# Kernel tuning notes

Hardware: AMD Instinct MI355X
Metric: run time of the kernel (lower is better)

The kernel has to match this reference:

```python
import jax, jax.numpy as jnp
import numpy as np

N_NODES = 100000
N_EDGES = 1600000
IN_CH = 256
HID = 64
N_FACTORS = 3
N_SKILLS = 7
NEG_SLOPE = 0.2  # PyG GATConv default leaky-relu slope


def setup_inputs() -> dict:
    key = jax.random.key(0)
    ks = jax.random.split(key, 16)
    def w(k, shape, fan_in):
        return jax.random.normal(k, shape, jnp.float32) * (1.0 / np.sqrt(fan_in))
    return {
        "x": jax.random.normal(ks[0], (N_NODES, IN_CH), jnp.float32),
        "edge_index": jax.random.randint(ks[1], (2, N_EDGES), 0, N_NODES, jnp.int32),
        # GAT layer 1
        "W1": w(ks[2], (IN_CH, HID), IN_CH),
        "a_src1": w(ks[3], (HID,), HID),
        "a_dst1": w(ks[4], (HID,), HID),
        "b1": jnp.zeros((HID,), jnp.float32),
        # GAT layer 2
        "W2": w(ks[5], (HID, HID), HID),
        "a_src2": w(ks[6], (HID,), HID),
        "a_dst2": w(ks[7], (HID,), HID),
        "b2": jnp.zeros((HID,), jnp.float32),
        # heads
        "Wf": w(ks[8], (HID, N_FACTORS), HID),
        "bf": jnp.zeros((N_FACTORS,), jnp.float32),
        "Ws": w(ks[9], (HID, N_SKILLS), HID),
        "bs": jnp.zeros((N_SKILLS,), jnp.float32),
    }


def _gat_layer(x, src, dst, W, a_src, a_dst, b):
    """Single-head GATConv (PyG defaults: heads=1, self-loops already appended)."""
    n = x.shape[0]
    h = x @ W                                     # [N, H] transformed features
    alpha_s = h @ a_src                           # [N] per-node source score
    alpha_d = h @ a_dst                           # [N] per-node destination score
    e = jax.nn.leaky_relu(alpha_s[src] + alpha_d[dst], NEG_SLOPE)  # [E]
    # numerically stable segment softmax over incoming edges of each dst node
    m = jax.ops.segment_max(e, dst, num_segments=n)
    w = jnp.exp(e - m[dst])
    den = jax.ops.segment_sum(w, dst, num_segments=n)
    alpha = w / den[dst]                          # [E] attention coefficients
    out = jax.ops.segment_sum(alpha[:, None] * h[src], dst, num_segments=n)
    return out + b


def reference(x, edge_index, W1, a_src1, a_dst1, b1, W2, a_src2, a_dst2, b2, Wf, bf, Ws, bs):
    n = x.shape[0]
    # GATConv default add_self_loops=True
    loops = jnp.arange(n, dtype=edge_index.dtype)
    src = jnp.concatenate([edge_index[0], loops])
    dst = jnp.concatenate([edge_index[1], loops])

    h = jax.nn.relu(_gat_layer(x, src, dst, W1, a_src1, a_dst1, b1))
    # dropout is identity in eval mode
    h = jax.nn.relu(_gat_layer(h, src, dst, W2, a_src2, a_dst2, b2))

    factors_logits = h @ Wf + bf   # [N, 3]
    skills_logits = h @ Ws + bs    # [N, 7]
    return (factors_logits, skills_logits)
```

## Files before the change

kernel.cpp:

```cpp
#include <hip/hip_runtime.h>

__global__ __launch_bounds__(256) void init_deg(int* deg, int N) {
    int i = blockIdx.x * blockDim.x + threadIdx.x;
    if (i < N) deg[i] = 1;
}

__global__ __launch_bounds__(256) void count_deg_r(const int* __restrict__ edst,
                                                   int* __restrict__ deg, int E,
                                                   float inv, int per_chunk) {
    int r = blockIdx.x & 7;
    int chunk = blockIdx.x >> 3;
    int base = chunk * per_chunk;
    int end = min(E, base + per_chunk);
    for (int e = base + (int)threadIdx.x; e < end; e += 256) {
        int d = edst[e];
        int reg = (int)((float)d * inv); reg = reg > 7 ? 7 : reg;
        if (reg == r) atomicAdd(&deg[d], 1);
    }
}

__global__ __launch_bounds__(256) void scan_pass1(const int* __restrict__ deg,
                                                  int* __restrict__ partials, int N) {
    __shared__ int sd[256];
    int b = blockIdx.x, t = threadIdx.x;
    int base = b * 1024 + t * 4;
    int s = 0;
#pragma unroll
    for (int k = 0; k < 4; k++) s += (base + k < N) ? deg[base + k] : 0;
    sd[t] = s; __syncthreads();
    for (int off = 1; off < 256; off <<= 1) {
        int v = (t >= off) ? sd[t - off] : 0;
        __syncthreads();
        sd[t] += v;
        __syncthreads();
    }
    if (t == 255) partials[b] = sd[255];
}

__global__ __launch_bounds__(256) void scan_pass2(int* __restrict__ partials, int nblk) {
    __shared__ int sd[256];
    int t = threadIdx.x;
    int v[4]; int s = 0;
#pragma unroll
    for (int k = 0; k < 4; k++) { int i = t * 4 + k; v[k] = (i < nblk) ? partials[i] : 0; s += v[k]; }
    sd[t] = s; __syncthreads();
    for (int off = 1; off < 256; off <<= 1) {
        int x = (t >= off) ? sd[t - off] : 0;
        __syncthreads();
        sd[t] += x;
        __syncthreads();
    }
    int run = sd[t] - s;
#pragma unroll
    for (int k = 0; k < 4; k++) { int i = t * 4 + k; if (i < nblk) partials[i] = run; run += v[k]; }
}

__global__ __launch_bounds__(256) void scan_pass3(const int* __restrict__ deg,
                                                  const int* __restrict__ partials,
                                                  int* __restrict__ rowstart, int N) {
    __shared__ int sd[256];
    int b = blockIdx.x, t = threadIdx.x;
    int base = b * 1024 + t * 4;
    int v[4]; int s = 0;
#pragma unroll
    for (int k = 0; k < 4; k++) { v[k] = (base + k < N) ? deg[base + k] : 0; s += v[k]; }
    sd[t] = s; __syncthreads();
    for (int off = 1; off < 256; off <<= 1) {
        int x = (t >= off) ? sd[t - off] : 0;
        __syncthreads();
        sd[t] += x;
        __syncthreads();
    }
    int run = partials[b] + sd[t] - s;
#pragma unroll
    for (int k = 0; k < 4; k++) { if (base + k < N) rowstart[base + k] = run; run += v[k]; }
}

__global__ __launch_bounds__(256) void scatter_r(const int* __restrict__ esrc,
                                                 const int* __restrict__ edst,
                                                 int* __restrict__ cursor,
                                                 int* __restrict__ sorted_src,
                                                 int E, int total, float inv, int per_chunk) {
    int r = blockIdx.x & 7;
    int chunk = blockIdx.x >> 3;
    int base = chunk * per_chunk;
    int end = min(total, base + per_chunk);
    for (int e = base + (int)threadIdx.x; e < end; e += 256) {
        int s, d;
        if (e < E) { s = esrc[e]; d = edst[e]; }
        else       { s = e - E;   d = s;       }
        int reg = (int)((float)d * inv); reg = reg > 7 ? 7 : reg;
        if (reg == r) {
            int pos = atomicAdd(&cursor[d], 1);
            sorted_src[pos] = s;
        }
    }
}

__global__ __launch_bounds__(256) void gemm_alpha(const float* __restrict__ A,
                                                  const float* __restrict__ W,
                                                  const float* __restrict__ a_src,
                                                  const float* __restrict__ a_dst,
                                                  float* __restrict__ C,
                                                  float* __restrict__ as_,
                                                  float* __restrict__ ad_,
                                                  int M, int K) {
    const int BK = 32;
    __shared__ float AsT[BK][132];
    __shared__ float Bs[BK][64];
    int tid = threadIdx.x;
    int tx = tid & 7;
    int ty = tid >> 3;
    int rowBase = blockIdx.x * 128;
    float acc[4][8] = {};

    float asv[8], adv[8];
#pragma unroll
    for (int j = 0; j < 8; j++) { asv[j] = a_src[tx * 8 + j]; adv[j] = a_dst[tx * 8 + j]; }

    for (int k0 = 0; k0 < K; k0 += BK) {
#pragma unroll
        for (int i = 0; i < 4; i++) {
            int fidx = 4 * (tid + i * 256);
            int r = fidx >> 5, c = fidx & 31;
            int gr = rowBase + r;
            float4 v = (gr < M) ? *reinterpret_cast<const float4*>(&A[(size_t)gr * K + k0 + c])
                                : make_float4(0.f, 0.f, 0.f, 0.f);
            AsT[c + 0][r] = v.x;
            AsT[c + 1][r] = v.y;
            AsT[c + 2][r] = v.z;
            AsT[c + 3][r] = v.w;
        }
#pragma unroll
        for (int i = 0; i < 2; i++) {
            int fidx = 4 * (tid + i * 256);
            int r = fidx >> 6, c = fidx & 63;
            *reinterpret_cast<float4*>(&Bs[r][c]) =
                *reinterpret_cast<const float4*>(&W[(size_t)(k0 + r) * 64 + c]);
        }
        __syncthreads();
#pragma unroll 4
        for (int kk = 0; kk < BK; ++kk) {
            float a[4], b[8];
            *reinterpret_cast<float4*>(&a[0]) = *reinterpret_cast<const float4*>(&AsT[kk][ty * 4]);
            *reinterpret_cast<float4*>(&b[0]) = *reinterpret_cast<const float4*>(&Bs[kk][tx * 8]);
            *reinterpret_cast<float4*>(&b[4]) = *reinterpret_cast<const float4*>(&Bs[kk][tx * 8 + 4]);
#pragma unroll
            for (int i = 0; i < 4; i++)
#pragma unroll
                for (int j = 0; j < 8; j++)
                    acc[i][j] += a[i] * b[j];
        }
        __syncthreads();
    }

#pragma unroll
    for (int i = 0; i < 4; i++) {
        int gr = rowBase + ty * 4 + i;
        float s1 = 0.f, s2 = 0.f;
#pragma unroll
        for (int j = 0; j < 8; j++) { s1 += acc[i][j] * asv[j]; s2 += acc[i][j] * adv[j]; }
        s1 += __shfl_xor(s1, 1); s2 += __shfl_xor(s2, 1);
        s1 += __shfl_xor(s1, 2); s2 += __shfl_xor(s2, 2);
        s1 += __shfl_xor(s1, 4); s2 += __shfl_xor(s2, 4);
        if (gr < M) {
            *reinterpret_cast<float4*>(&C[(size_t)gr * 64 + tx * 8]) =
                make_float4(acc[i][0], acc[i][1], acc[i][2], acc[i][3]);
            *reinterpret_cast<float4*>(&C[(size_t)gr * 64 + tx * 8 + 4]) =
                make_float4(acc[i][4], acc[i][5], acc[i][6], acc[i][7]);
            if (tx == 0) { as_[gr] = s1; ad_[gr] = s2; }
        }
    }
}

__global__ __launch_bounds__(256) void aggregate_kernel(const float* __restrict__ h,
                                                        const float* __restrict__ as_,
                                                        const float* __restrict__ ad_,
                                                        const int* __restrict__ rowstart,
                                                        const int* __restrict__ sorted_src,
                                                        const float* __restrict__ bias,
                                                        float* __restrict__ outp,
                                                        int N, int total) {
    int wid = (blockIdx.x * blockDim.x + threadIdx.x) >> 6;
    int lane = threadIdx.x & 63;
    if (wid >= N) return;
    int beg = rowstart[wid];
    int end = (wid + 1 < N) ? rowstart[wid + 1] : total;
    float a_d = ad_[wid];
    float acc = 0.f, den = 0.f;
    int j = beg;
    for (; j + 3 < end; j += 4) {
        int s0 = sorted_src[j],     s1 = sorted_src[j + 1];
        int s2 = sorted_src[j + 2], s3 = sorted_src[j + 3];
        float e0 = as_[s0] + a_d, e1 = as_[s1] + a_d;
        float e2 = as_[s2] + a_d, e3 = as_[s3] + a_d;
        e0 = e0 > 0.f ? e0 : 0.2f * e0;
        e1 = e1 > 0.f ? e1 : 0.2f * e1;
        e2 = e2 > 0.f ? e2 : 0.2f * e2;
        e3 = e3 > 0.f ? e3 : 0.2f * e3;
        float w0 = __expf(e0), w1 = __expf(e1), w2 = __expf(e2), w3 = __expf(e3);
        float h0 = h[(size_t)s0 * 64 + lane];
        float h1 = h[(size_t)s1 * 64 + lane];
        float h2 = h[(size_t)s2 * 64 + lane];
        float h3 = h[(size_t)s3 * 64 + lane];
        den += (w0 + w1) + (w2 + w3);
        acc += (w0 * h0 + w1 * h1) + (w2 * h2 + w3 * h3);
    }
    for (; j < end; j++) {
        int s0 = sorted_src[j];
        float e0 = as_[s0] + a_d;
        e0 = e0 > 0.f ? e0 : 0.2f * e0;
        float w0 = __expf(e0);
        den += w0;
        acc += w0 * h[(size_t)s0 * 64 + lane];
    }
    float v = acc / den + bias[lane];
    outp[(size_t)wid * 64 + lane] = v > 0.f ? v : 0.f;
}

__global__ __launch_bounds__(256) void aggregate_heads(const float* __restrict__ h,
                                                       const float* __restrict__ as_,
                                                       const float* __restrict__ ad_,
                                                       const int* __restrict__ rowstart,
                                                       const int* __restrict__ sorted_src,
                                                       const float* __restrict__ bias,
                                                       const float* __restrict__ Wf,
                                                       const float* __restrict__ bf,
                                                       const float* __restrict__ Ws,
                                                       const float* __restrict__ bs,
                                                       float* __restrict__ out,
                                                       int N, int total) {
    int wid = (blockIdx.x * blockDim.x + threadIdx.x) >> 6;
    int lane = threadIdx.x & 63;
    if (wid >= N) return;
    int beg = rowstart[wid];
    int end = (wid + 1 < N) ? rowstart[wid + 1] : total;
    float a_d = ad_[wid];
    float acc = 0.f, den = 0.f;
    int j = beg;
    for (; j + 3 < end; j += 4) {
        int s0 = sorted_src[j],     s1 = sorted_src[j + 1];
        int s2 = sorted_src[j + 2], s3 = sorted_src[j + 3];
        float e0 = as_[s0] + a_d, e1 = as_[s1] + a_d;
        float e2 = as_[s2] + a_d, e3 = as_[s3] + a_d;
        e0 = e0 > 0.f ? e0 : 0.2f * e0;
        e1 = e1 > 0.f ? e1 : 0.2f * e1;
        e2 = e2 > 0.f ? e2 : 0.2f * e2;
        e3 = e3 > 0.f ? e3 : 0.2f * e3;
        float w0 = __expf(e0), w1 = __expf(e1), w2 = __expf(e2), w3 = __expf(e3);
        float h0 = h[(size_t)s0 * 64 + lane];
        float h1 = h[(size_t)s1 * 64 + lane];
        float h2 = h[(size_t)s2 * 64 + lane];
        float h3 = h[(size_t)s3 * 64 + lane];
        den += (w0 + w1) + (w2 + w3);
        acc += (w0 * h0 + w1 * h1) + (w2 * h2 + w3 * h3);
    }
    for (; j < end; j++) {
        int s0 = sorted_src[j];
        float e0 = as_[s0] + a_d;
        e0 = e0 > 0.f ? e0 : 0.2f * e0;
        float w0 = __expf(e0);
        den += w0;
        acc += w0 * h[(size_t)s0 * 64 + lane];
    }
    float v = acc / den + bias[lane];
    v = v > 0.f ? v : 0.f;
#pragma unroll
    for (int q = 0; q < 3; q++) {
        float p = v * Wf[lane * 3 + q];
#pragma unroll
        for (int off = 32; off; off >>= 1) p += __shfl_xor(p, off);
        if (lane == 0) out[(size_t)wid * 3 + q] = p + bf[q];
    }
#pragma unroll
    for (int q = 0; q < 7; q++) {
        float p = v * Ws[lane * 7 + q];
#pragma unroll
        for (int off = 32; off; off >>= 1) p += __shfl_xor(p, off);
        if (lane == 0) out[(size_t)N * 3 + (size_t)wid * 7 + q] = p + bs[q];
    }
}

extern "C" void kernel_launch(void* const* d_in, const int* in_sizes, int n_in,
                              void* d_out, int out_size, void* d_ws, size_t ws_size,
                              hipStream_t stream) {
    const float* x      = (const float*)d_in[0];
    const int*   ei     = (const int*)  d_in[1];
    const float* W1     = (const float*)d_in[2];
    const float* a_src1 = (const float*)d_in[3];
    const float* a_dst1 = (const float*)d_in[4];
    const float* b1     = (const float*)d_in[5];
    const float* W2     = (const float*)d_in[6];
    const float* a_src2 = (const float*)d_in[7];
    const float* a_dst2 = (const float*)d_in[8];
    const float* b2     = (const float*)d_in[9];
    const float* Wf     = (const float*)d_in[10];
    const float* bf     = (const float*)d_in[11];
    const float* Ws     = (const float*)d_in[12];
    const float* bs     = (const float*)d_in[13];
    float* out = (float*)d_out;

    const int IN = 256;
    int N = in_sizes[0] / IN;
    int E = in_sizes[1] / 2;
    int total = E + N;

    char* ws = (char*)d_ws;
    float* h        = (float*)ws;  ws += (size_t)N * 64 * sizeof(float);
    float* g        = (float*)ws;  ws += (size_t)N * 64 * sizeof(float);
    float* as_      = (float*)ws;  ws += (size_t)N * sizeof(float);
    float* ad_      = (float*)ws;  ws += (size_t)N * sizeof(float);
    int* rowstart   = (int*)ws;    ws += (size_t)(N + 1) * sizeof(int);
    int* cursor     = (int*)ws;    ws += (size_t)N * sizeof(int);
    int* sorted_src = (int*)ws;    ws += (size_t)total * sizeof(int);
    int* partials   = (int*)ws;    ws += 1024 * sizeof(int);

    const int* esrc = ei;
    const int* edst = ei + E;

    float inv = 8.0f / (float)N;
    int nblk = (N + 1023) / 1024;
    int gemmGrid = (N + 127) / 128;
    int aggGrid  = (N * 64 + 255) / 256;
    int pcE = (E + 255) / 256;
    int pcT = (total + 255) / 256;

    init_deg<<<(N + 255) / 256, 256, 0, stream>>>(cursor, N);
    count_deg_r<<<2048, 256, 0, stream>>>(edst, cursor, E, inv, pcE);
    scan_pass1<<<nblk, 256, 0, stream>>>(cursor, partials, N);
    scan_pass2<<<1, 256, 0, stream>>>(partials, nblk);
    scan_pass3<<<nblk, 256, 0, stream>>>(cursor, partials, rowstart, N);
    hipMemcpyAsync(cursor, rowstart, (size_t)N * sizeof(int), hipMemcpyDeviceToDevice, stream);
    scatter_r<<<2048, 256, 0, stream>>>(esrc, edst, cursor, sorted_src, E, total, inv, pcT);

    gemm_alpha<<<gemmGrid, 256, 0, stream>>>(x, W1, a_src1, a_dst1, h, as_, ad_, N, IN);
    aggregate_kernel<<<aggGrid, 256, 0, stream>>>(h, as_, ad_, rowstart, sorted_src, b1, g, N, total);

    gemm_alpha<<<gemmGrid, 256, 0, stream>>>(g, W2, a_src2, a_dst2, h, as_, ad_, N, 64);
    aggregate_heads<<<aggGrid, 256, 0, stream>>>(h, as_, ad_, rowstart, sorted_src, b2,
                                                 Wf, bf, Ws, bs, out, N, total);
}
```

Before: 592.4 us.

## Store transformed features in fp16 and handle self-loops inline in aggregation

GEMM output h is written as half precision and converted back to float in the gather-heavy aggregation kernels, halving feature gather bandwidth. Self-loops are no longer materialized in the CSR; each aggregation computes the self-edge term directly, removing the init kernel, the device memcpy, and N extra scatter entries. The cursor is now zeroed by memset and filled alongside rowstart in the scan. The fp16 storage reduces precision of intermediate features, which risks exceeding the accuracy tolerance.

```diff
diff --git a/kernel.cpp b/kernel.cpp
--- a/kernel.cpp
+++ b/kernel.cpp
@@ -1,9 +1,5 @@
 #include <hip/hip_runtime.h>
-
-__global__ __launch_bounds__(256) void init_deg(int* deg, int N) {
-    int i = blockIdx.x * blockDim.x + threadIdx.x;
-    if (i < N) deg[i] = 1;
-}
+#include <hip/hip_fp16.h>
 
 __global__ __launch_bounds__(256) void count_deg_r(const int* __restrict__ edst,
                                                    int* __restrict__ deg, int E,
@@ -57,7 +53,8 @@
 
 __global__ __launch_bounds__(256) void scan_pass3(const int* __restrict__ deg,
                                                   const int* __restrict__ partials,
-                                                  int* __restrict__ rowstart, int N) {
+                                                  int* __restrict__ rowstart,
+                                                  int* __restrict__ cursor, int N) {
     __shared__ int sd[256];
     int b = blockIdx.x, t = threadIdx.x;
     int base = b * 1024 + t * 4;
@@ -73,22 +70,23 @@
     }
     int run = partials[b] + sd[t] - s;
 #pragma unroll
-    for (int k = 0; k < 4; k++) { if (base + k < N) rowstart[base + k] = run; run += v[k]; }
+    for (int k = 0; k < 4; k++) {
+        if (base + k < N) { rowstart[base + k] = run; cursor[base + k] = run; }
+        run += v[k];
+    }
 }
 
 __global__ __launch_bounds__(256) void scatter_r(const int* __restrict__ esrc,
                                                  const int* __restrict__ edst,
                                                  int* __restrict__ cursor,
                                                  int* __restrict__ sorted_src,
-                                                 int E, int total, float inv, int per_chunk) {
+                                                 int E, float inv, int per_chunk) {
     int r = blockIdx.x & 7;
     int chunk = blockIdx.x >> 3;
     int base = chunk * per_chunk;
-    int end = min(total, base + per_chunk);
+    int end = min(E, base + per_chunk);
     for (int e = base + (int)threadIdx.x; e < end; e += 256) {
-        int s, d;
-        if (e < E) { s = esrc[e]; d = edst[e]; }
-        else       { s = e - E;   d = s;       }
+        int s = esrc[e], d = edst[e];
         int reg = (int)((float)d * inv); reg = reg > 7 ? 7 : reg;
         if (reg == r) {
             int pos = atomicAdd(&cursor[d], 1);
@@ -101,7 +99,7 @@
                                                   const float* __restrict__ W,
                                                   const float* __restrict__ a_src,
                                                   const float* __restrict__ a_dst,
-                                                  float* __restrict__ C,
+                                                  __half* __restrict__ C,
                                                   float* __restrict__ as_,
                                                   float* __restrict__ ad_,
                                                   int M, int K) {
@@ -164,30 +162,35 @@
         s1 += __shfl_xor(s1, 2); s2 += __shfl_xor(s2, 2);
         s1 += __shfl_xor(s1, 4); s2 += __shfl_xor(s2, 4);
         if (gr < M) {
+            __half hb[8];
+#pragma unroll
+            for (int j = 0; j < 8; j++) hb[j] = __float2half(acc[i][j]);
             *reinterpret_cast<float4*>(&C[(size_t)gr * 64 + tx * 8]) =
-                make_float4(acc[i][0], acc[i][1], acc[i][2], acc[i][3]);
-            *reinterpret_cast<float4*>(&C[(size_t)gr * 64 + tx * 8 + 4]) =
-                make_float4(acc[i][4], acc[i][5], acc[i][6], acc[i][7]);
+                *reinterpret_cast<const float4*>(&hb[0]);
             if (tx == 0) { as_[gr] = s1; ad_[gr] = s2; }
         }
     }
 }
 
-__global__ __launch_bounds__(256) void aggregate_kernel(const float* __restrict__ h,
+__global__ __launch_bounds__(256) void aggregate_kernel(const __half* __restrict__ h,
                                                         const float* __restrict__ as_,
                                                         const float* __restrict__ ad_,
                                                         const int* __restrict__ rowstart,
                                                         const int* __restrict__ sorted_src,
                                                         const float* __restrict__ bias,
                                                         float* __restrict__ outp,
-                                                        int N, int total) {
+                                                        int N, int E) {
     int wid = (blockIdx.x * blockDim.x + threadIdx.x) >> 6;
     int lane = threadIdx.x & 63;
     if (wid >= N) return;
     int beg = rowstart[wid];
-    int end = (wid + 1 < N) ? rowstart[wid + 1] : total;
+    int end = (wid + 1 < N) ? rowstart[wid + 1] : E;
     float a_d = ad_[wid];
-    float acc = 0.f, den = 0.f;
+    float es = as_[wid] + a_d;
+    es = es > 0.f ? es : 0.2f * es;
+    float wself = __expf(es);
+    float den = wself;
+    float acc = wself * __half2float(h[(size_t)wid * 64 + lane]);
     int j = beg;
     for (; j + 3 < end; j += 4) {
         int s0 = sorted_src[j],     s1 = sorted_src[j + 1];
@@ -199,10 +202,10 @@
         e2 = e2 > 0.f ? e2 : 0.2f * e2;
         e3 = e3 > 0.f ? e3 : 0.2f * e3;
         float w0 = __expf(e0), w1 = __expf(e1), w2 = __expf(e2), w3 = __expf(e3);
-        float h0 = h[(size_t)s0 * 64 + lane];
-        float h1 = h[(size_t)s1 * 64 + lane];
-        float h2 = h[(size_t)s2 * 64 + lane];
-        float h3 = h[(size_t)s3 * 64 + lane];
+        float h0 = __half2float(h[(size_t)s0 * 64 + lane]);
+        float h1 = __half2float(h[(size_t)s1 * 64 + lane]);
+        float h2 = __half2float(h[(size_t)s2 * 64 + lane]);
+        float h3 = __half2float(h[(size_t)s3 * 64 + lane]);
         den += (w0 + w1) + (w2 + w3);
         acc += (w0 * h0 + w1 * h1) + (w2 * h2 + w3 * h3);
     }
@@ -212,13 +215,13 @@
         e0 = e0 > 0.f ? e0 : 0.2f * e0;
         float w0 = __expf(e0);
         den += w0;
-        acc += w0 * h[(size_t)s0 * 64 + lane];
+        acc += w0 * __half2float(h[(size_t)s0 * 64 + lane]);
     }
     float v = acc / den + bias[lane];
     outp[(size_t)wid * 64 + lane] = v > 0.f ? v : 0.f;
 }
 
-__global__ __launch_bounds__(256) void aggregate_heads(const float* __restrict__ h,
+__global__ __launch_bounds__(256) void aggregate_heads(const __half* __restrict__ h,
                                                        const float* __restrict__ as_,
                                                        const float* __restrict__ ad_,
                                                        const int* __restrict__ rowstart,
@@ -229,14 +232,18 @@
                                                        const float* __restrict__ Ws,
                                                        const float* __restrict__ bs,
                                                        float* __restrict__ out,
-                                                       int N, int total) {
+                                                       int N, int E) {
     int wid = (blockIdx.x * blockDim.x + threadIdx.x) >> 6;
     int lane = threadIdx.x & 63;
     if (wid >= N) return;
     int beg = rowstart[wid];
-    int end = (wid + 1 < N) ? rowstart[wid + 1] : total;
+    int end = (wid + 1 < N) ? rowstart[wid + 1] : E;
     float a_d = ad_[wid];
-    float acc = 0.f, den = 0.f;
+    float es = as_[wid] + a_d;
+    es = es > 0.f ? es : 0.2f * es;
+    float wself = __expf(es);
+    float den = wself;
+    float acc = wself * __half2float(h[(size_t)wid * 64 + lane]);
     int j = beg;
     for (; j + 3 < end; j += 4) {
         int s0 = sorted_src[j],     s1 = sorted_src[j + 1];
@@ -248,10 +255,10 @@
         e2 = e2 > 0.f ? e2 : 0.2f * e2;
         e3 = e3 > 0.f ? e3 : 0.2f * e3;
         float w0 = __expf(e0), w1 = __expf(e1), w2 = __expf(e2), w3 = __expf(e3);
-        float h0 = h[(size_t)s0 * 64 + lane];
-        float h1 = h[(size_t)s1 * 64 + lane];
-        float h2 = h[(size_t)s2 * 64 + lane];
-        float h3 = h[(size_t)s3 * 64 + lane];
+        float h0 = __half2float(h[(size_t)s0 * 64 + lane]);
+        float h1 = __half2float(h[(size_t)s1 * 64 + lane]);
+        float h2 = __half2float(h[(size_t)s2 * 64 + lane]);
+        float h3 = __half2float(h[(size_t)s3 * 64 + lane]);
         den += (w0 + w1) + (w2 + w3);
         acc += (w0 * h0 + w1 * h1) + (w2 * h2 + w3 * h3);
     }
@@ -261,7 +268,7 @@
         e0 = e0 > 0.f ? e0 : 0.2f * e0;
         float w0 = __expf(e0);
         den += w0;
-        acc += w0 * h[(size_t)s0 * 64 + lane];
+        acc += w0 * __half2float(h[(size_t)s0 * 64 + lane]);
     }
     float v = acc / den + bias[lane];
     v = v > 0.f ? v : 0.f;
@@ -303,16 +310,15 @@
     const int IN = 256;
     int N = in_sizes[0] / IN;
     int E = in_sizes[1] / 2;
-    int total = E + N;
 
     char* ws = (char*)d_ws;
-    float* h        = (float*)ws;  ws += (size_t)N * 64 * sizeof(float);
+    __half* h       = (__half*)ws; ws += (size_t)N * 64 * sizeof(__half);
     float* g        = (float*)ws;  ws += (size_t)N * 64 * sizeof(float);
     float* as_      = (float*)ws;  ws += (size_t)N * sizeof(float);
     float* ad_      = (float*)ws;  ws += (size_t)N * sizeof(float);
     int* rowstart   = (int*)ws;    ws += (size_t)(N + 1) * sizeof(int);
     int* cursor     = (int*)ws;    ws += (size_t)N * sizeof(int);
-    int* sorted_src = (int*)ws;    ws += (size_t)total * sizeof(int);
+    int* sorted_src = (int*)ws;    ws += (size_t)E * sizeof(int);
     int* partials   = (int*)ws;    ws += 1024 * sizeof(int);
 
     const int* esrc = ei;
@@ -323,20 +329,18 @@
     int gemmGrid = (N + 127) / 128;
     int aggGrid  = (N * 64 + 255) / 256;
     int pcE = (E + 255) / 256;
-    int pcT = (total + 255) / 256;
-
-    init_deg<<<(N + 255) / 256, 256, 0, stream>>>(cursor, N);
+
+    hipMemsetAsync(cursor, 0, (size_t)N * sizeof(int), stream);
     count_deg_r<<<2048, 256, 0, stream>>>(edst, cursor, E, inv, pcE);
     scan_pass1<<<nblk, 256, 0, stream>>>(cursor, partials, N);
     scan_pass2<<<1, 256, 0, stream>>>(partials, nblk);
-    scan_pass3<<<nblk, 256, 0, stream>>>(cursor, partials, rowstart, N);
-    hipMemcpyAsync(cursor, rowstart, (size_t)N * sizeof(int), hipMemcpyDeviceToDevice, stream);
-    scatter_r<<<2048, 256, 0, stream>>>(esrc, edst, cursor, sorted_src, E, total, inv, pcT);
+    scan_pass3<<<nblk, 256, 0, stream>>>(cursor, partials, rowstart, cursor, N);
+    scatter_r<<<2048, 256, 0, stream>>>(esrc, edst, cursor, sorted_src, E, inv, pcE);
 
     gemm_alpha<<<gemmGrid, 256, 0, stream>>>(x, W1, a_src1, a_dst1, h, as_, ad_, N, IN);
-    aggregate_kernel<<<aggGrid, 256, 0, stream>>>(h, as_, ad_, rowstart, sorted_src, b1, g, N, total);
+    aggregate_kernel<<<aggGrid, 256, 0, stream>>>(h, as_, ad_, rowstart, sorted_src, b1, g, N, E);
 
     gemm_alpha<<<gemmGrid, 256, 0, stream>>>(g, W2, a_src2, a_dst2, h, as_, ad_, N, 64);
     aggregate_heads<<<aggGrid, 256, 0, stream>>>(h, as_, ad_, rowstart, sorted_src, b2,
-                                                 Wf, bf, Ws, bs, out, N, total);
-}
+                                                 Wf, bf, Ws, bs, out, N, E);
+}
```

Measured after the change: 570.2 us. 1.04x faster.
